# Performance work log

Measured on AMD Instinct MI355X. Metric: run time of the kernel, lower is better.

## Reference

```python
import jax, jax.numpy as jnp
import numpy as np

B, T_E, T_D, H = 32, 128, 128, 256  # batch, encoder len, decoder len, hidden


def lstm_scan(x, h0, c0, Wih, Whh, bih, bhh):
    """Single-layer PyTorch-style LSTM over x: [B, T, F] -> (hs, cs) each [T, B, H]."""
    bias = bih + bhh

    def step(carry, xt):
        h, c = carry
        gates = xt @ Wih.T + h @ Whh.T + bias  # [B, 4H], gate order i,f,g,o
        i, f, g, o = jnp.split(gates, 4, axis=-1)
        i = jax.nn.sigmoid(i)
        f = jax.nn.sigmoid(f)
        o = jax.nn.sigmoid(o)
        g = jnp.tanh(g)
        c = f * c + i * g
        h = o * jnp.tanh(c)
        return (h, c), (h, c)

    _, (hs, cs) = jax.lax.scan(step, (h0, c0), jnp.swapaxes(x, 0, 1))
    return hs, cs


def setup_inputs() -> dict:
    key = jax.random.key(0)
    ks = jax.random.split(key, 16)
    seq = jax.random.normal(ks[0], (B, T_E), jnp.float32)
    seq_m = jax.random.randint(ks[1], (B, 1), 1, T_E + 1)  # valid lengths in [1, T_E]
    pos = jnp.arange(T_E)[None, :]
    seq = jnp.where(pos < seq_m, seq, 0.0)  # zero-pad beyond length (drives the mask)
    target = jax.random.normal(ks[2], (B, T_D), jnp.float32)

    s = 0.1
    nrm = lambda k, shape: s * jax.random.normal(k, shape, jnp.float32)
    return dict(
        seq=seq, seq_m=seq_m, target=target,
        Wih_e=nrm(ks[3], (4 * H, 1)), Whh_e=nrm(ks[4], (4 * H, H)),
        bih_e=nrm(ks[5], (4 * H,)), bhh_e=nrm(ks[6], (4 * H,)),
        Wih_d=nrm(ks[7], (4 * H, 1)), Whh_d=nrm(ks[8], (4 * H, H)),
        bih_d=nrm(ks[9], (4 * H,)), bhh_d=nrm(ks[10], (4 * H,)),
        We=nrm(ks[11], (H, H)), be=nrm(ks[12], (H,)),
        Wd=nrm(ks[13], (H, H)), bd=nrm(ks[14], (H,)),
        v=jnp.ones((H,), jnp.float32),
    )


def reference(seq, seq_m, target,
              Wih_e, Whh_e, bih_e, bhh_e,
              Wih_d, Whh_d, bih_d, bhh_d,
              We, be, Wd, bd, v):
    zeros = jnp.zeros((B, H), seq.dtype)
    # Encoder: one fused scan instead of the original per-timestep Python loop
    hs_e, cs_e = lstm_scan(seq[..., None], zeros, zeros, Wih_e, Whh_e, bih_e, bhh_e)
    e = jnp.swapaxes(hs_e, 0, 1)  # [B, T_E, H]

    # Grab encoder state at the last valid step (seq_m - 1) per batch element
    last = seq_m[:, 0] - 1  # [B]
    bidx = jnp.arange(B)
    e_hs = hs_e[last, bidx]  # [B, H]
    e_cs = cs_e[last, bidx]

    # Decoder initialized from the selected encoder state
    hs_d, _ = lstm_scan(target[..., None], e_hs, e_cs, Wih_d, Whh_d, bih_d, bhh_d)
    d = jnp.swapaxes(hs_d, 0, 1)  # [B, T_D, H]

    e2 = e @ We.T + be  # [B, T_E, H]
    d2 = d @ Wd.T + bd  # [B, T_D, H]

    # Additive (Bahdanau) attention: tanh(e_j + d_i) . v  -> [B, T_D, T_E]
    t = jnp.tanh(d2[:, :, None, :] + e2[:, None, :, :])  # [B, T_D, T_E, H]
    p = jnp.einsum('bijh,h->bij', t, v)

    # Masking: original sets seq[:,0]=0.1 then adds 1000 where seq value nonzero,
    # after subtracting 1000 everywhere -> padded (zero) positions end up at -1000.
    seq0 = seq.at[:, 0].set(0.1)
    mask = (seq0 != 0).astype(p.dtype)  # [B, T_E]
    p = p + (mask[:, None, :] - 1.0) * 1000.0

    return jax.nn.softmax(p, axis=-1)  # pointer distribution over encoder positions
```

## Files before the change

kernel.cpp:

```cpp
#include <hip/hip_runtime.h>
#include <hip/hip_bf16.h>

#define BB 32
#define TT 128
#define HH 256
#define G4 4
#define UPB 64
#define RPB 256

#define AGENT __HIP_MEMORY_SCOPE_AGENT
#define AL(p) __hip_atomic_load((p), __ATOMIC_RELAXED, AGENT)

__device__ __forceinline__ float rcp_f(float x) { return __builtin_amdgcn_rcpf(x); }
__device__ __forceinline__ float sigmoid_f(float x) {
    return rcp_f(1.f + __expf(-x));
}
__device__ __forceinline__ float tanh_f(float x) {
    float e = __expf(2.f * x);
    return 1.f - 2.f * rcp_f(e + 1.f);
}

__global__ __launch_bounds__(256) void prep_transpose(
    const float* __restrict__ We, const float* __restrict__ Wd,
    float* __restrict__ WeT, float* __restrict__ WdT) {
    __shared__ float t[64][65];
    const int m = blockIdx.x >> 4;
    const int tile = blockIdx.x & 15;
    const float* S = m ? Wd : We;
    float* D = m ? WdT : WeT;
    const int r0 = (tile >> 2) * 64, c0 = (tile & 3) * 64;
    const int lr = threadIdx.x >> 4;
    const int lc = threadIdx.x & 15;
    for (int rr = lr; rr < 64; rr += 16)
        *(float4*)&t[rr][lc * 4] = *(const float4*)&S[(r0 + rr) * HH + c0 + lc * 4];
    __syncthreads();
    for (int rr = lr; rr < 64; rr += 16) {
        float4 v;
        v.x = t[lc * 4 + 0][rr];
        v.y = t[lc * 4 + 1][rr];
        v.z = t[lc * 4 + 2][rr];
        v.w = t[lc * 4 + 3][rr];
        *(float4*)&D[(c0 + rr) * HH + r0 + lc * 4] = v;
    }
}

__global__ __launch_bounds__(512, 2) void lstm_kernel(
    const float* __restrict__ seq,
    const int* __restrict__ seq_m,
    const float* __restrict__ target,
    const float* __restrict__ Wih_e,
    const float* __restrict__ Whh_e,
    const float* __restrict__ bih_e, const float* __restrict__ bhh_e,
    const float* __restrict__ Wih_d, const float* __restrict__ Whh_d,
    const float* __restrict__ bih_d, const float* __restrict__ bhh_d,
    float* __restrict__ e_out,
    float* __restrict__ d_out,
    unsigned long long* __restrict__ mbox,
    unsigned long long* __restrict__ hsave)
{
    const int blk = blockIdx.x;
    const int b = blk & 31;
    const int g = blk >> 5;
    const int tid = threadIdx.x;
    const int wave = tid >> 6;
    const int lane = tid & 63;
    const int half = wave & 1;
    const int row = (wave >> 1) * 64 + lane;
    const int gate = row >> 6;
    const int u_local = row & 63;
    const int row_global = gate * HH + g * UPB + u_local;
    const int last = seq_m[b] - 1;

    __shared__ float h_lds[HH];
    __shared__ float g_lds[2 * RPB];
    __shared__ float bias_lds[RPB];
    __shared__ float wih_lds[RPB];
    __shared__ float x_lds[2 * TT];

    for (int i = tid; i < TT; i += 512) {
        x_lds[i] = seq[b * TT + i];
        x_lds[TT + i] = target[b * TT + i];
    }

    float4 w[32];
    auto loadw = [&](const float* Whh, const float* Wih,
                     const float* bih, const float* bhh) {
        const float4* wr = (const float4*)(Whh + row_global * HH + half * 128);
#pragma unroll
        for (int i = 0; i < 32; ++i) w[i] = wr[i];
        if (half == 0) {
            bias_lds[row] = bih[row_global] + bhh[row_global];
            wih_lds[row] = Wih[row_global];
        }
    };
    loadw(Whh_e, Wih_e, bih_e, bhh_e);

    if (tid < 64) ((float4*)h_lds)[tid] = make_float4(0.f, 0.f, 0.f, 0.f);
    __syncthreads();

    float c = 0.f, c_saved = 0.f, h_saved = 0.f;

    for (int t = 0; t < 2 * TT; ++t) {
        const int phase = t >> 7;
        const int tt = t & 127;

        const float4* h4 = (const float4*)(h_lds + (half << 7));
        float4 a4 = make_float4(0.f, 0.f, 0.f, 0.f);
#pragma unroll
        for (int i = 0; i < 32; ++i) {
            float4 hv = h4[i];
            a4.x = fmaf(w[i].x, hv.x, a4.x);
            a4.y = fmaf(w[i].y, hv.y, a4.y);
            a4.z = fmaf(w[i].z, hv.z, a4.z);
            a4.w = fmaf(w[i].w, hv.w, a4.w);
        }
        g_lds[(half << 8) + row] = (a4.x + a4.y) + (a4.z + a4.w);
        __syncthreads();

        if (tid < 64) {
            const float x = x_lds[t];
            float gi = g_lds[tid] + g_lds[256 + tid] + bias_lds[tid] +
                       x * wih_lds[tid];
            float gf = g_lds[64 + tid] + g_lds[320 + tid] + bias_lds[64 + tid] +
                       x * wih_lds[64 + tid];
            float gg = g_lds[128 + tid] + g_lds[384 + tid] + bias_lds[128 + tid] +
                       x * wih_lds[128 + tid];
            float go = g_lds[192 + tid] + g_lds[448 + tid] + bias_lds[192 + tid] +
                       x * wih_lds[192 + tid];
            float si = sigmoid_f(gi);
            float sf = sigmoid_f(gf);
            float tg = tanh_f(gg);
            float so = sigmoid_f(go);
            c = sf * c + si * tg;
            float h = so * tanh_f(c);
            const int ug = g * UPB + tid;
            unsigned long long pkt =
                ((unsigned long long)(unsigned)(t + 1) << 32) | __float_as_uint(h);
            __hip_atomic_store(&mbox[(t & 1) * BB * HH + b * HH + ug], pkt,
                               __ATOMIC_RELAXED, AGENT);
            if (phase == 0 && tt == last) {
                c_saved = c;
                h_saved = h;
                unsigned long long spkt =
                    (1ull << 32) | (unsigned long long)__float_as_uint(h);
                __hip_atomic_store(&hsave[b * HH + ug], spkt, __ATOMIC_RELAXED, AGENT);
            }
            h_lds[ug] = (t == TT - 1) ? h_saved : h;
            (phase ? d_out : e_out)[(b * TT + tt) * HH + ug] = h;
        }

        if (tid >= 64 && tid < 256) {
            const int p = (g + (tid >> 6)) & 3;
            const int pl = tid & 63;
            const int pu = p * UPB + pl;
            unsigned long long* src;
            unsigned want;
            if (t == TT - 1) {
                src = &hsave[b * HH + pu];
                want = 1u;
            } else {
                src = &mbox[(t & 1) * BB * HH + b * HH + pu];
                want = (unsigned)(t + 1);
            }
            unsigned long long pv;
            {
                unsigned long long r0 = AL(src);
                __builtin_amdgcn_s_sleep(3);
                unsigned long long r1 = AL(src);
                __builtin_amdgcn_s_sleep(3);
                unsigned long long r2 = AL(src);
                __builtin_amdgcn_s_sleep(3);
                unsigned long long r3 = AL(src);
                for (;;) {
                    if ((unsigned)(r0 >> 32) == want) { pv = r0; break; }
                    r0 = AL(src);
                    if ((unsigned)(r1 >> 32) == want) { pv = r1; break; }
                    r1 = AL(src);
                    if ((unsigned)(r2 >> 32) == want) { pv = r2; break; }
                    r2 = AL(src);
                    if ((unsigned)(r3 >> 32) == want) { pv = r3; break; }
                    r3 = AL(src);
                }
            }
            h_lds[pu] = __uint_as_float((unsigned)pv);
        }
        __syncthreads();

        if (t == TT - 1) {
            loadw(Whh_d, Wih_d, bih_d, bhh_d);
            c = c_saved;
        }
    }
}

__global__ __launch_bounds__(256) void proj_kernel(
    const float* __restrict__ e_in, const float* __restrict__ d_in,
    const float* __restrict__ WeT, const float* __restrict__ WdT,
    const float* __restrict__ be, const float* __restrict__ bd,
    float* __restrict__ e2, float* __restrict__ d2) {
    __shared__ float tile[16][HH];
    const int blk = blockIdx.x;
    const bool isd = blk >= 256;
    const float* in = isd ? d_in : e_in;
    const float* WT = isd ? WdT : WeT;
    const float* bias = isd ? bd : be;
    float* out = isd ? d2 : e2;
    const int r0 = (isd ? blk - 256 : blk) * 16;
    const int tid = threadIdx.x;

    {
        const float4* src = (const float4*)(in + r0 * HH);
        float4* dst = (float4*)(&tile[0][0]);
        for (int idx = tid; idx < 16 * 64; idx += 256) dst[idx] = src[idx];
    }
    __syncthreads();

    float acc[16];
#pragma unroll
    for (int r = 0; r < 16; ++r) acc[r] = 0.f;
    const int cidx = tid;
    for (int k = 0; k < HH; k += 4) {
        float w0 = WT[(k + 0) * HH + cidx];
        float w1 = WT[(k + 1) * HH + cidx];
        float w2 = WT[(k + 2) * HH + cidx];
        float w3 = WT[(k + 3) * HH + cidx];
#pragma unroll
        for (int r = 0; r < 16; ++r) {
            float4 iv = *(const float4*)&tile[r][k];
            acc[r] = fmaf(iv.x, w0, acc[r]);
            acc[r] = fmaf(iv.y, w1, acc[r]);
            acc[r] = fmaf(iv.z, w2, acc[r]);
            acc[r] = fmaf(iv.w, w3, acc[r]);
        }
    }
    const float bb = bias[cidx];
#pragma unroll
    for (int r = 0; r < 16; ++r) out[(r0 + r) * HH + cidx] = acc[r] + bb;
}

#define EPAD 260
#define PPAD 132
__global__ __launch_bounds__(256) void attn_kernel(
    const float* __restrict__ e2, const float* __restrict__ d2,
    const float* __restrict__ vv, const float* __restrict__ seq,
    float* __restrict__ out) {
    __shared__ float e2c[32][EPAD];
    __shared__ float d2t[32][EPAD];
    __shared__ float p_lds[32][PPAD];
    __shared__ float v_lds[HH];

    const int blk = blockIdx.x;
    const int b = blk >> 2;
    const int i0 = (blk & 3) * 32;
    const int tid = threadIdx.x;
    const int jl = tid & 31, ig = tid >> 5;

    if (tid < 64) *(float4*)&v_lds[tid * 4] = ((const float4*)vv)[tid];
    for (int idx = tid; idx < 32 * 64; idx += 256) {
        int r = idx >> 6, q = idx & 63;
        *(float4*)&d2t[r][q * 4] = ((const float4*)(d2 + (b * TT + i0 + r) * HH))[q];
    }

    for (int jc = 0; jc < TT; jc += 32) {
        __syncthreads();
        for (int idx = tid; idx < 32 * 64; idx += 256) {
            int r = idx >> 6, q = idx & 63;
            *(float4*)&e2c[r][q * 4] = ((const float4*)(e2 + (b * TT + jc + r) * HH))[q];
        }
        __syncthreads();

        float a0 = 0.f, a1 = 0.f, a2 = 0.f, a3 = 0.f;
        for (int h = 0; h < HH; h += 4) {
            float4 ev = *(const float4*)&e2c[jl][h];
            float4 vx = *(const float4*)&v_lds[h];
            float4 d0 = *(const float4*)&d2t[ig * 4 + 0][h];
            float4 d1 = *(const float4*)&d2t[ig * 4 + 1][h];
            float4 d2v = *(const float4*)&d2t[ig * 4 + 2][h];
            float4 d3 = *(const float4*)&d2t[ig * 4 + 3][h];
            a0 = fmaf(tanh_f(ev.x + d0.x), vx.x, a0);
            a0 = fmaf(tanh_f(ev.y + d0.y), vx.y, a0);
            a0 = fmaf(tanh_f(ev.z + d0.z), vx.z, a0);
            a0 = fmaf(tanh_f(ev.w + d0.w), vx.w, a0);
            a1 = fmaf(tanh_f(ev.x + d1.x), vx.x, a1);
            a1 = fmaf(tanh_f(ev.y + d1.y), vx.y, a1);
            a1 = fmaf(tanh_f(ev.z + d1.z), vx.z, a1);
            a1 = fmaf(tanh_f(ev.w + d1.w), vx.w, a1);
            a2 = fmaf(tanh_f(ev.x + d2v.x), vx.x, a2);
            a2 = fmaf(tanh_f(ev.y + d2v.y), vx.y, a2);
            a2 = fmaf(tanh_f(ev.z + d2v.z), vx.z, a2);
            a2 = fmaf(tanh_f(ev.w + d2v.w), vx.w, a2);
            a3 = fmaf(tanh_f(ev.x + d3.x), vx.x, a3);
            a3 = fmaf(tanh_f(ev.y + d3.y), vx.y, a3);
            a3 = fmaf(tanh_f(ev.z + d3.z), vx.z, a3);
            a3 = fmaf(tanh_f(ev.w + d3.w), vx.w, a3);
        }
        const int j = jc + jl;
        float sv = (j == 0) ? 0.1f : seq[b * TT + j];
        float msk = (sv == 0.f) ? -1000.f : 0.f;
        p_lds[ig * 4 + 0][j] = a0 + msk;
        p_lds[ig * 4 + 1][j] = a1 + msk;
        p_lds[ig * 4 + 2][j] = a2 + msk;
        p_lds[ig * 4 + 3][j] = a3 + msk;
    }
    __syncthreads();

    const int r = tid >> 3, l8 = tid & 7;
    float xr[16];
    float m = -1e30f;
#pragma unroll
    for (int k = 0; k < 16; ++k) {
        xr[k] = p_lds[r][l8 + 8 * k];
        m = fmaxf(m, xr[k]);
    }
#pragma unroll
    for (int o = 4; o >= 1; o >>= 1) m = fmaxf(m, __shfl_xor(m, o));
    float s = 0.f;
#pragma unroll
    for (int k = 0; k < 16; ++k) {
        xr[k] = __expf(xr[k] - m);
        s += xr[k];
    }
#pragma unroll
    for (int o = 4; o >= 1; o >>= 1) s += __shfl_xor(s, o);
    float inv = rcp_f(s);
    float* orow = out + (b * TT + i0 + r) * TT;
#pragma unroll
    for (int k = 0; k < 16; ++k) orow[l8 + 8 * k] = xr[k] * inv;
}

extern "C" void kernel_launch(void* const* d_in, const int* in_sizes, int n_in,
                              void* d_out, int out_size, void* d_ws, size_t ws_size,
                              hipStream_t stream) {
    const float* seq = (const float*)d_in[0];
    const int* seq_m = (const int*)d_in[1];
    const float* target = (const float*)d_in[2];
    const float* Wih_e = (const float*)d_in[3];
    const float* Whh_e = (const float*)d_in[4];
    const float* bih_e = (const float*)d_in[5];
    const float* bhh_e = (const float*)d_in[6];
    const float* Wih_d = (const float*)d_in[7];
    const float* Whh_d = (const float*)d_in[8];
    const float* bih_d = (const float*)d_in[9];
    const float* bhh_d = (const float*)d_in[10];
    const float* We = (const float*)d_in[11];
    const float* be = (const float*)d_in[12];
    const float* Wd = (const float*)d_in[13];
    const float* bd = (const float*)d_in[14];
    const float* vv = (const float*)d_in[15];

    float* ws = (float*)d_ws;
    const size_t SZ_ED = (size_t)BB * TT * HH;
    float* e_buf = ws;
    float* d_buf = e_buf + SZ_ED;
    float* e2 = d_buf + SZ_ED;
    float* d2 = e2 + SZ_ED;
    float* WeT = d2 + SZ_ED;
    float* WdT = WeT + HH * HH;
    unsigned long long* mbox = (unsigned long long*)(WdT + HH * HH);
    unsigned long long* hsave = mbox + 2 * BB * HH;

    const size_t needed = (4 * SZ_ED + 2 * HH * HH) * sizeof(float) +
                          3 * BB * HH * sizeof(unsigned long long);
    if (ws_size < needed) return;

    hipMemsetAsync(mbox, 0, 3 * BB * HH * sizeof(unsigned long long), stream);
    prep_transpose<<<32, 256, 0, stream>>>(We, Wd, WeT, WdT);
    lstm_kernel<<<BB * G4, 512, 0, stream>>>(seq, seq_m, target, Wih_e, Whh_e, bih_e,
                                             bhh_e, Wih_d, Whh_d, bih_d, bhh_d, e_buf,
                                             d_buf, mbox, hsave);
    proj_kernel<<<512, 256, 0, stream>>>(e_buf, d_buf, WeT, WdT, be, bd, e2, d2);
    attn_kernel<<<BB * 4, 256, 0, stream>>>(e2, d2, vv, seq, (float*)d_out);
}
```

Measured before the change: 695.6 us.

## Batch four sequences per LSTM block and pipeline cross-block exchange across them

Each LSTM block now handles four batch elements with the same register-resident weight slice, shrinking the grid from 128 to 32 blocks. Within a timestep it processes the sequences one after another, and while one sequence computes its gates, helper threads poll the mailbox for another sequence's hidden state from peer blocks. This is meant to hide inter-block communication latency behind useful work. The half-row dot-product split also moves to adjacent lanes reduced with a shuffle, and bias and input weights move into registers. The cost is four times the serial work per block, twice the number of __syncthreads per step, and fewer CUs in use.

```diff
diff --git a/kernel.cpp b/kernel.cpp
--- a/kernel.cpp
+++ b/kernel.cpp
@@ -4,9 +4,9 @@
 #define BB 32
 #define TT 128
 #define HH 256
-#define G4 4
 #define UPB 64
 #define RPB 256
+#define NQ 4
 
 #define AGENT __HIP_MEMORY_SCOPE_AGENT
 #define AL(p) __hip_atomic_load((p), __ATOMIC_RELAXED, AGENT)
@@ -59,136 +59,140 @@
     unsigned long long* __restrict__ hsave)
 {
     const int blk = blockIdx.x;
-    const int b = blk & 31;
-    const int g = blk >> 5;
+    const int g = blk & 3;
+    const int b0 = (blk >> 2) * NQ;
     const int tid = threadIdx.x;
-    const int wave = tid >> 6;
-    const int lane = tid & 63;
-    const int half = wave & 1;
-    const int row = (wave >> 1) * 64 + lane;
-    const int gate = row >> 6;
-    const int u_local = row & 63;
+    const int row_local = tid >> 1;
+    const int half = tid & 1;
+    const int gate = row_local >> 6;
+    const int u_local = row_local & 63;
     const int row_global = gate * HH + g * UPB + u_local;
-    const int last = seq_m[b] - 1;
-
-    __shared__ float h_lds[HH];
-    __shared__ float g_lds[2 * RPB];
-    __shared__ float bias_lds[RPB];
-    __shared__ float wih_lds[RPB];
-    __shared__ float x_lds[2 * TT];
-
-    for (int i = tid; i < TT; i += 512) {
-        x_lds[i] = seq[b * TT + i];
-        x_lds[TT + i] = target[b * TT + i];
-    }
+
+    __shared__ float h_lds[NQ][HH];
+    __shared__ float g_lds[RPB];
+    __shared__ float x_lds[NQ][2 * TT];
+
+    for (int i = tid; i < NQ * 2 * TT; i += 512) {
+        const int q = i >> 8, idx = i & 255;
+        x_lds[q][idx] = (idx < TT) ? seq[(b0 + q) * TT + idx]
+                                   : target[(b0 + q) * TT + (idx - TT)];
+    }
+
+    int last[NQ];
+#pragma unroll
+    for (int q = 0; q < NQ; ++q) last[q] = seq_m[b0 + q] - 1;
 
     float4 w[32];
+    float bias_r, wih_r;
     auto loadw = [&](const float* Whh, const float* Wih,
                      const float* bih, const float* bhh) {
         const float4* wr = (const float4*)(Whh + row_global * HH + half * 128);
 #pragma unroll
         for (int i = 0; i < 32; ++i) w[i] = wr[i];
-        if (half == 0) {
-            bias_lds[row] = bih[row_global] + bhh[row_global];
-            wih_lds[row] = Wih[row_global];
-        }
+        bias_r = bih[row_global] + bhh[row_global];
+        wih_r = Wih[row_global];
     };
     loadw(Whh_e, Wih_e, bih_e, bhh_e);
 
-    if (tid < 64) ((float4*)h_lds)[tid] = make_float4(0.f, 0.f, 0.f, 0.f);
+    for (int i = tid; i < NQ * 64; i += 512)
+        ((float4*)&h_lds[0][0])[i] = make_float4(0.f, 0.f, 0.f, 0.f);
     __syncthreads();
 
-    float c = 0.f, c_saved = 0.f, h_saved = 0.f;
+    float c[NQ], c_saved[NQ], h_saved[NQ];
+#pragma unroll
+    for (int q = 0; q < NQ; ++q) { c[q] = 0.f; c_saved[q] = 0.f; h_saved[q] = 0.f; }
 
     for (int t = 0; t < 2 * TT; ++t) {
         const int phase = t >> 7;
         const int tt = t & 127;
-
-        const float4* h4 = (const float4*)(h_lds + (half << 7));
-        float4 a4 = make_float4(0.f, 0.f, 0.f, 0.f);
-#pragma unroll
-        for (int i = 0; i < 32; ++i) {
-            float4 hv = h4[i];
-            a4.x = fmaf(w[i].x, hv.x, a4.x);
-            a4.y = fmaf(w[i].y, hv.y, a4.y);
-            a4.z = fmaf(w[i].z, hv.z, a4.z);
-            a4.w = fmaf(w[i].w, hv.w, a4.w);
-        }
-        g_lds[(half << 8) + row] = (a4.x + a4.y) + (a4.z + a4.w);
-        __syncthreads();
-
-        if (tid < 64) {
-            const float x = x_lds[t];
-            float gi = g_lds[tid] + g_lds[256 + tid] + bias_lds[tid] +
-                       x * wih_lds[tid];
-            float gf = g_lds[64 + tid] + g_lds[320 + tid] + bias_lds[64 + tid] +
-                       x * wih_lds[64 + tid];
-            float gg = g_lds[128 + tid] + g_lds[384 + tid] + bias_lds[128 + tid] +
-                       x * wih_lds[128 + tid];
-            float go = g_lds[192 + tid] + g_lds[448 + tid] + bias_lds[192 + tid] +
-                       x * wih_lds[192 + tid];
-            float si = sigmoid_f(gi);
-            float sf = sigmoid_f(gf);
-            float tg = tanh_f(gg);
-            float so = sigmoid_f(go);
-            c = sf * c + si * tg;
-            float h = so * tanh_f(c);
-            const int ug = g * UPB + tid;
-            unsigned long long pkt =
-                ((unsigned long long)(unsigned)(t + 1) << 32) | __float_as_uint(h);
-            __hip_atomic_store(&mbox[(t & 1) * BB * HH + b * HH + ug], pkt,
-                               __ATOMIC_RELAXED, AGENT);
-            if (phase == 0 && tt == last) {
-                c_saved = c;
-                h_saved = h;
-                unsigned long long spkt =
-                    (1ull << 32) | (unsigned long long)__float_as_uint(h);
-                __hip_atomic_store(&hsave[b * HH + ug], spkt, __ATOMIC_RELAXED, AGENT);
+#pragma unroll
+        for (int q = 0; q < NQ; ++q) {
+            const float4* h4 = ((const float4*)&h_lds[q][0]) + half * 32;
+            float4 a4 = make_float4(0.f, 0.f, 0.f, 0.f);
+#pragma unroll
+            for (int i = 0; i < 32; ++i) {
+                float4 hv = h4[i];
+                a4.x = fmaf(w[i].x, hv.x, a4.x);
+                a4.y = fmaf(w[i].y, hv.y, a4.y);
+                a4.z = fmaf(w[i].z, hv.z, a4.z);
+                a4.w = fmaf(w[i].w, hv.w, a4.w);
             }
-            h_lds[ug] = (t == TT - 1) ? h_saved : h;
-            (phase ? d_out : e_out)[(b * TT + tt) * HH + ug] = h;
-        }
-
-        if (tid >= 64 && tid < 256) {
-            const int p = (g + (tid >> 6)) & 3;
-            const int pl = tid & 63;
-            const int pu = p * UPB + pl;
-            unsigned long long* src;
-            unsigned want;
-            if (t == TT - 1) {
-                src = &hsave[b * HH + pu];
-                want = 1u;
-            } else {
-                src = &mbox[(t & 1) * BB * HH + b * HH + pu];
-                want = (unsigned)(t + 1);
+            float acc = (a4.x + a4.y) + (a4.z + a4.w);
+            acc += __shfl_xor(acc, 1);
+            float gv = acc + bias_r + x_lds[q][t] * wih_r;
+            if (half == 0) g_lds[row_local] = gv;
+            __syncthreads();
+
+            if (tid < 64) {
+                float gi = g_lds[tid];
+                float gf = g_lds[64 + tid];
+                float gg = g_lds[128 + tid];
+                float go = g_lds[192 + tid];
+                float si = sigmoid_f(gi);
+                float sf = sigmoid_f(gf);
+                float tg = tanh_f(gg);
+                float so = sigmoid_f(go);
+                c[q] = sf * c[q] + si * tg;
+                float h = so * tanh_f(c[q]);
+                const int ug = g * UPB + tid;
+                const int b = b0 + q;
+                unsigned long long pkt =
+                    ((unsigned long long)(unsigned)(t + 1) << 32) | __float_as_uint(h);
+                __hip_atomic_store(&mbox[(t & 1) * BB * HH + b * HH + ug], pkt,
+                                   __ATOMIC_RELAXED, AGENT);
+                if (phase == 0 && tt == last[q]) {
+                    c_saved[q] = c[q];
+                    h_saved[q] = h;
+                    unsigned long long spkt =
+                        (1ull << 32) | (unsigned long long)__float_as_uint(h);
+                    __hip_atomic_store(&hsave[b * HH + ug], spkt, __ATOMIC_RELAXED,
+                                       AGENT);
+                }
+                h_lds[q][ug] = (t == TT - 1) ? h_saved[q] : h;
+                (phase ? d_out : e_out)[(b * TT + tt) * HH + ug] = h;
             }
-            unsigned long long pv;
-            {
-                unsigned long long r0 = AL(src);
-                __builtin_amdgcn_s_sleep(3);
-                unsigned long long r1 = AL(src);
-                __builtin_amdgcn_s_sleep(3);
-                unsigned long long r2 = AL(src);
-                __builtin_amdgcn_s_sleep(3);
-                unsigned long long r3 = AL(src);
-                for (;;) {
-                    if ((unsigned)(r0 >> 32) == want) { pv = r0; break; }
-                    r0 = AL(src);
-                    if ((unsigned)(r1 >> 32) == want) { pv = r1; break; }
-                    r1 = AL(src);
-                    if ((unsigned)(r2 >> 32) == want) { pv = r2; break; }
-                    r2 = AL(src);
-                    if ((unsigned)(r3 >> 32) == want) { pv = r3; break; }
-                    r3 = AL(src);
+
+            if (tid >= 64 && tid < 256) {
+                const int p = (q + 1) & 3;
+                const int tp = (q == 3) ? t : t - 1;
+                if (tp >= 0 && tp < 2 * TT - 1) {
+                    const int pr = (g + (tid >> 6)) & 3;
+                    const int lane = tid & 63;
+                    const int pu = pr * UPB + lane;
+                    unsigned long long* src;
+                    unsigned want;
+                    if (tp == TT - 1) {
+                        src = &hsave[(b0 + p) * HH + pu];
+                        want = 1u;
+                    } else {
+                        src = &mbox[(tp & 1) * BB * HH + (b0 + p) * HH + pu];
+                        want = (unsigned)(tp + 1);
+                    }
+                    unsigned long long pv;
+                    unsigned long long r0 = AL(src);
+                    unsigned long long r1 = AL(src);
+                    unsigned long long r2 = AL(src);
+                    unsigned long long r3 = AL(src);
+                    for (;;) {
+                        if ((unsigned)(r0 >> 32) == want) { pv = r0; break; }
+                        r0 = AL(src);
+                        if ((unsigned)(r1 >> 32) == want) { pv = r1; break; }
+                        r1 = AL(src);
+                        if ((unsigned)(r2 >> 32) == want) { pv = r2; break; }
+                        r2 = AL(src);
+                        if ((unsigned)(r3 >> 32) == want) { pv = r3; break; }
+                        r3 = AL(src);
+                    }
+                    h_lds[p][pu] = __uint_as_float((unsigned)pv);
                 }
             }
-            h_lds[pu] = __uint_as_float((unsigned)pv);
-        }
-        __syncthreads();
+            __syncthreads();
+        }
 
         if (t == TT - 1) {
             loadw(Whh_d, Wih_d, bih_d, bhh_d);
-            c = c_saved;
+#pragma unroll
+            for (int q = 0; q < NQ; ++q) c[q] = c_saved[q];
         }
     }
 }
@@ -365,9 +369,9 @@
 
     hipMemsetAsync(mbox, 0, 3 * BB * HH * sizeof(unsigned long long), stream);
     prep_transpose<<<32, 256, 0, stream>>>(We, Wd, WeT, WdT);
-    lstm_kernel<<<BB * G4, 512, 0, stream>>>(seq, seq_m, target, Wih_e, Whh_e, bih_e,
-                                             bhh_e, Wih_d, Whh_d, bih_d, bhh_d, e_buf,
-                                             d_buf, mbox, hsave);
+    lstm_kernel<<<32, 512, 0, stream>>>(seq, seq_m, target, Wih_e, Whh_e, bih_e,
+                                        bhh_e, Wih_d, Whh_d, bih_d, bhh_d, e_buf,
+                                        d_buf, mbox, hsave);
     proj_kernel<<<512, 256, 0, stream>>>(e_buf, d_buf, WeT, WdT, be, bd, e2, d2);
     attn_kernel<<<BB * 4, 256, 0, stream>>>(e2, d2, vv, seq, (float*)d_out);
 }
```

Measured after the change: 1.735 ms. 149% more time.

## Fuse encoder/decoder output projections into LSTM recurrence kernel

Applied to the files above, without the earlier changes.

Removes the separate transpose and projection kernels and computes e2/d2 inside the LSTM kernel. Idle threads (tid>=256) project the previous step's full hidden state with register-resident We/Wd rows while the next step runs. The kernel also reorganizes the gate matvec so adjacent lanes split K and reduce via shuffle, with bias and input terms folded in per row. It double-buffers h in LDS and drops the s_sleep in the polling loop. This avoids writing and rereading the e/d hidden sequences and two launches, at the cost of more register pressure and extra work per recurrent step.

```diff
diff --git a/kernel.cpp b/kernel.cpp
--- a/kernel.cpp
+++ b/kernel.cpp
@@ -18,30 +18,6 @@
 __device__ __forceinline__ float tanh_f(float x) {
     float e = __expf(2.f * x);
     return 1.f - 2.f * rcp_f(e + 1.f);
-}
-
-__global__ __launch_bounds__(256) void prep_transpose(
-    const float* __restrict__ We, const float* __restrict__ Wd,
-    float* __restrict__ WeT, float* __restrict__ WdT) {
-    __shared__ float t[64][65];
-    const int m = blockIdx.x >> 4;
-    const int tile = blockIdx.x & 15;
-    const float* S = m ? Wd : We;
-    float* D = m ? WdT : WeT;
-    const int r0 = (tile >> 2) * 64, c0 = (tile & 3) * 64;
-    const int lr = threadIdx.x >> 4;
-    const int lc = threadIdx.x & 15;
-    for (int rr = lr; rr < 64; rr += 16)
-        *(float4*)&t[rr][lc * 4] = *(const float4*)&S[(r0 + rr) * HH + c0 + lc * 4];
-    __syncthreads();
-    for (int rr = lr; rr < 64; rr += 16) {
-        float4 v;
-        v.x = t[lc * 4 + 0][rr];
-        v.y = t[lc * 4 + 1][rr];
-        v.z = t[lc * 4 + 2][rr];
-        v.w = t[lc * 4 + 3][rr];
-        *(float4*)&D[(c0 + rr) * HH + r0 + lc * 4] = v;
-    }
 }
 
 __global__ __launch_bounds__(512, 2) void lstm_kernel(
@@ -53,8 +29,10 @@
     const float* __restrict__ bih_e, const float* __restrict__ bhh_e,
     const float* __restrict__ Wih_d, const float* __restrict__ Whh_d,
     const float* __restrict__ bih_d, const float* __restrict__ bhh_d,
-    float* __restrict__ e_out,
-    float* __restrict__ d_out,
+    const float* __restrict__ We, const float* __restrict__ be,
+    const float* __restrict__ Wd, const float* __restrict__ bd,
+    float* __restrict__ e2,
+    float* __restrict__ d2,
     unsigned long long* __restrict__ mbox,
     unsigned long long* __restrict__ hsave)
 {
@@ -62,20 +40,21 @@
     const int b = blk & 31;
     const int g = blk >> 5;
     const int tid = threadIdx.x;
-    const int wave = tid >> 6;
-    const int lane = tid & 63;
-    const int half = wave & 1;
-    const int row = (wave >> 1) * 64 + lane;
-    const int gate = row >> 6;
-    const int u_local = row & 63;
+    const int row_local = tid >> 1;
+    const int half = tid & 1;
+    const int gate = row_local >> 6;
+    const int u_local = row_local & 63;
     const int row_global = gate * HH + g * UPB + u_local;
     const int last = seq_m[b] - 1;
-
-    __shared__ float h_lds[HH];
-    __shared__ float g_lds[2 * RPB];
-    __shared__ float bias_lds[RPB];
-    __shared__ float wih_lds[RPB];
+    const int s = tid - 256;
+    const int pu = s >> 2;
+    const int kq = s & 3;
+    const int pcol = g * UPB + pu;
+
+    __shared__ float hbuf[2][HH];
+    __shared__ float g_lds[RPB];
     __shared__ float x_lds[2 * TT];
+    __shared__ float h_final[HH];
 
     for (int i = tid; i < TT; i += 512) {
         x_lds[i] = seq[b * TT + i];
@@ -83,19 +62,30 @@
     }
 
     float4 w[32];
+    float bias_r, wih_r;
     auto loadw = [&](const float* Whh, const float* Wih,
                      const float* bih, const float* bhh) {
         const float4* wr = (const float4*)(Whh + row_global * HH + half * 128);
 #pragma unroll
         for (int i = 0; i < 32; ++i) w[i] = wr[i];
-        if (half == 0) {
-            bias_lds[row] = bih[row_global] + bhh[row_global];
-            wih_lds[row] = Wih[row_global];
-        }
+        bias_r = bih[row_global] + bhh[row_global];
+        wih_r = Wih[row_global];
     };
     loadw(Whh_e, Wih_e, bih_e, bhh_e);
 
-    if (tid < 64) ((float4*)h_lds)[tid] = make_float4(0.f, 0.f, 0.f, 0.f);
+    float4 pw[16];
+    float pb = 0.f;
+    auto loadp = [&](const float* W, const float* bias) {
+        const float4* src = (const float4*)(W + pcol * HH + kq * 64);
+#pragma unroll
+        for (int i = 0; i < 16; ++i) pw[i] = src[i];
+        pb = bias[pcol];
+    };
+    if (tid >= 256) loadp(We, be);
+
+    if (tid < 64) {
+        ((float4*)hbuf[1])[tid] = make_float4(0.f, 0.f, 0.f, 0.f);
+    }
     __syncthreads();
 
     float c = 0.f, c_saved = 0.f, h_saved = 0.f;
@@ -103,8 +93,10 @@
     for (int t = 0; t < 2 * TT; ++t) {
         const int phase = t >> 7;
         const int tt = t & 127;
-
-        const float4* h4 = (const float4*)(h_lds + (half << 7));
+        const float x = x_lds[t];
+        const int rb = (t & 1) ^ 1;
+
+        const float4* h4 = ((const float4*)hbuf[rb]) + half * 32;
         float4 a4 = make_float4(0.f, 0.f, 0.f, 0.f);
 #pragma unroll
         for (int i = 0; i < 32; ++i) {
@@ -114,19 +106,17 @@
             a4.z = fmaf(w[i].z, hv.z, a4.z);
             a4.w = fmaf(w[i].w, hv.w, a4.w);
         }
-        g_lds[(half << 8) + row] = (a4.x + a4.y) + (a4.z + a4.w);
+        float acc = (a4.x + a4.y) + (a4.z + a4.w);
+        acc += __shfl_xor(acc, 1);
+        float gv = acc + bias_r + x * wih_r;
+        if (half == 0) g_lds[row_local] = gv;
         __syncthreads();
 
         if (tid < 64) {
-            const float x = x_lds[t];
-            float gi = g_lds[tid] + g_lds[256 + tid] + bias_lds[tid] +
-                       x * wih_lds[tid];
-            float gf = g_lds[64 + tid] + g_lds[320 + tid] + bias_lds[64 + tid] +
-                       x * wih_lds[64 + tid];
-            float gg = g_lds[128 + tid] + g_lds[384 + tid] + bias_lds[128 + tid] +
-                       x * wih_lds[128 + tid];
-            float go = g_lds[192 + tid] + g_lds[448 + tid] + bias_lds[192 + tid] +
-                       x * wih_lds[192 + tid];
+            float gi = g_lds[tid];
+            float gf = g_lds[64 + tid];
+            float gg = g_lds[128 + tid];
+            float go = g_lds[192 + tid];
             float si = sigmoid_f(gi);
             float sf = sigmoid_f(gf);
             float tg = tanh_f(gg);
@@ -145,31 +135,27 @@
                     (1ull << 32) | (unsigned long long)__float_as_uint(h);
                 __hip_atomic_store(&hsave[b * HH + ug], spkt, __ATOMIC_RELAXED, AGENT);
             }
-            h_lds[ug] = (t == TT - 1) ? h_saved : h;
-            (phase ? d_out : e_out)[(b * TT + tt) * HH + ug] = h;
+            hbuf[t & 1][ug] = (t == TT - 1) ? h_saved : h;
         }
 
         if (tid >= 64 && tid < 256) {
             const int p = (g + (tid >> 6)) & 3;
-            const int pl = tid & 63;
-            const int pu = p * UPB + pl;
+            const int lane = tid & 63;
+            const int ppu = p * UPB + lane;
             unsigned long long* src;
             unsigned want;
             if (t == TT - 1) {
-                src = &hsave[b * HH + pu];
+                src = &hsave[b * HH + ppu];
                 want = 1u;
             } else {
-                src = &mbox[(t & 1) * BB * HH + b * HH + pu];
+                src = &mbox[(t & 1) * BB * HH + b * HH + ppu];
                 want = (unsigned)(t + 1);
             }
             unsigned long long pv;
             {
                 unsigned long long r0 = AL(src);
-                __builtin_amdgcn_s_sleep(3);
                 unsigned long long r1 = AL(src);
-                __builtin_amdgcn_s_sleep(3);
                 unsigned long long r2 = AL(src);
-                __builtin_amdgcn_s_sleep(3);
                 unsigned long long r3 = AL(src);
                 for (;;) {
                     if ((unsigned)(r0 >> 32) == want) { pv = r0; break; }
@@ -182,8 +168,46 @@
                     r3 = AL(src);
                 }
             }
-            h_lds[pu] = __uint_as_float((unsigned)pv);
-        }
+            hbuf[t & 1][ppu] = __uint_as_float((unsigned)pv);
+        }
+
+        if (tid >= 256 && t >= 1) {
+            const float* hsrc = (t == TT) ? h_final : hbuf[rb];
+            const float4* hp = (const float4*)(hsrc + kq * 64);
+            float pa = 0.f;
+#pragma unroll
+            for (int i = 0; i < 16; ++i) {
+                float4 hv = hp[i];
+                pa = fmaf(pw[i].x, hv.x, pa);
+                pa = fmaf(pw[i].y, hv.y, pa);
+                pa = fmaf(pw[i].z, hv.z, pa);
+                pa = fmaf(pw[i].w, hv.w, pa);
+            }
+            pa += __shfl_xor(pa, 1);
+            pa += __shfl_xor(pa, 2);
+            if (kq == 0) {
+                if (t <= TT)
+                    e2[(b * TT + (t - 1)) * HH + pcol] = pa + pb;
+                else
+                    d2[(b * TT + (t - 1 - TT)) * HH + pcol] = pa + pb;
+            }
+        }
+        if (tid >= 256 && t == TT - 1) {
+            unsigned long long* src = &mbox[((TT - 1) & 1) * BB * HH + b * HH + s];
+            const unsigned want = (unsigned)TT;
+            unsigned long long r0 = AL(src);
+            unsigned long long r1 = AL(src);
+            unsigned long long pv;
+            for (;;) {
+                if ((unsigned)(r0 >> 32) == want) { pv = r0; break; }
+                r0 = AL(src);
+                if ((unsigned)(r1 >> 32) == want) { pv = r1; break; }
+                r1 = AL(src);
+            }
+            h_final[s] = __uint_as_float((unsigned)pv);
+        }
+        if (tid >= 256 && t == TT) loadp(Wd, bd);
+
         __syncthreads();
 
         if (t == TT - 1) {
@@ -191,51 +215,37 @@
             c = c_saved;
         }
     }
-}
-
-__global__ __launch_bounds__(256) void proj_kernel(
-    const float* __restrict__ e_in, const float* __restrict__ d_in,
-    const float* __restrict__ WeT, const float* __restrict__ WdT,
-    const float* __restrict__ be, const float* __restrict__ bd,
-    float* __restrict__ e2, float* __restrict__ d2) {
-    __shared__ float tile[16][HH];
-    const int blk = blockIdx.x;
-    const bool isd = blk >= 256;
-    const float* in = isd ? d_in : e_in;
-    const float* WT = isd ? WdT : WeT;
-    const float* bias = isd ? bd : be;
-    float* out = isd ? d2 : e2;
-    const int r0 = (isd ? blk - 256 : blk) * 16;
-    const int tid = threadIdx.x;
-
-    {
-        const float4* src = (const float4*)(in + r0 * HH);
-        float4* dst = (float4*)(&tile[0][0]);
-        for (int idx = tid; idx < 16 * 64; idx += 256) dst[idx] = src[idx];
+
+    if (tid >= 256) {
+        unsigned long long* src = &mbox[((2 * TT - 1) & 1) * BB * HH + b * HH + s];
+        const unsigned want = (unsigned)(2 * TT);
+        unsigned long long r0 = AL(src);
+        unsigned long long r1 = AL(src);
+        unsigned long long pv;
+        for (;;) {
+            if ((unsigned)(r0 >> 32) == want) { pv = r0; break; }
+            r0 = AL(src);
+            if ((unsigned)(r1 >> 32) == want) { pv = r1; break; }
+            r1 = AL(src);
+        }
+        h_final[s] = __uint_as_float((unsigned)pv);
     }
     __syncthreads();
-
-    float acc[16];
-#pragma unroll
-    for (int r = 0; r < 16; ++r) acc[r] = 0.f;
-    const int cidx = tid;
-    for (int k = 0; k < HH; k += 4) {
-        float w0 = WT[(k + 0) * HH + cidx];
-        float w1 = WT[(k + 1) * HH + cidx];
-        float w2 = WT[(k + 2) * HH + cidx];
-        float w3 = WT[(k + 3) * HH + cidx];
-#pragma unroll
-        for (int r = 0; r < 16; ++r) {
-            float4 iv = *(const float4*)&tile[r][k];
-            acc[r] = fmaf(iv.x, w0, acc[r]);
-            acc[r] = fmaf(iv.y, w1, acc[r]);
-            acc[r] = fmaf(iv.z, w2, acc[r]);
-            acc[r] = fmaf(iv.w, w3, acc[r]);
-        }
-    }
-    const float bb = bias[cidx];
-#pragma unroll
-    for (int r = 0; r < 16; ++r) out[(r0 + r) * HH + cidx] = acc[r] + bb;
+    if (tid >= 256) {
+        const float4* hp = (const float4*)(h_final + kq * 64);
+        float pa = 0.f;
+#pragma unroll
+        for (int i = 0; i < 16; ++i) {
+            float4 hv = hp[i];
+            pa = fmaf(pw[i].x, hv.x, pa);
+            pa = fmaf(pw[i].y, hv.y, pa);
+            pa = fmaf(pw[i].z, hv.z, pa);
+            pa = fmaf(pw[i].w, hv.w, pa);
+        }
+        pa += __shfl_xor(pa, 1);
+        pa += __shfl_xor(pa, 2);
+        if (kq == 0) d2[(b * TT + (TT - 1)) * HH + pcol] = pa + pb;
+    }
 }
 
 #define EPAD 260
@@ -350,24 +360,18 @@
 
     float* ws = (float*)d_ws;
     const size_t SZ_ED = (size_t)BB * TT * HH;
-    float* e_buf = ws;
-    float* d_buf = e_buf + SZ_ED;
-    float* e2 = d_buf + SZ_ED;
+    float* e2 = ws;
     float* d2 = e2 + SZ_ED;
-    float* WeT = d2 + SZ_ED;
-    float* WdT = WeT + HH * HH;
-    unsigned long long* mbox = (unsigned long long*)(WdT + HH * HH);
+    unsigned long long* mbox = (unsigned long long*)(d2 + SZ_ED);
     unsigned long long* hsave = mbox + 2 * BB * HH;
 
-    const size_t needed = (4 * SZ_ED + 2 * HH * HH) * sizeof(float) +
-                          3 * BB * HH * sizeof(unsigned long long);
+    const size_t needed =
+        2 * SZ_ED * sizeof(float) + 3 * BB * HH * sizeof(unsigned long long);
     if (ws_size < needed) return;
 
     hipMemsetAsync(mbox, 0, 3 * BB * HH * sizeof(unsigned long long), stream);
-    prep_transpose<<<32, 256, 0, stream>>>(We, Wd, WeT, WdT);
     lstm_kernel<<<BB * G4, 512, 0, stream>>>(seq, seq_m, target, Wih_e, Whh_e, bih_e,
-                                             bhh_e, Wih_d, Whh_d, bih_d, bhh_d, e_buf,
-                                             d_buf, mbox, hsave);
-    proj_kernel<<<512, 256, 0, stream>>>(e_buf, d_buf, WeT, WdT, be, bd, e2, d2);
+                                             bhh_e, Wih_d, Whh_d, bih_d, bhh_d, We,
+                                             be, Wd, bd, e2, d2, mbox, hsave);
     attn_kernel<<<BB * 4, 256, 0, stream>>>(e2, d2, vv, seq, (float*)d_out);
 }
```

New measurement: 647.2 us. 7.0% less time.
